# Optimization experiments

Measured on AMD Instinct MI355X. Metric: run time of the kernel, lower is better.

Reference implementation:

```python
import jax, jax.numpy as jnp
import numpy as np

NUM_USERS = 10000
NUM_ITEMS = 100000
EMBED_DIM = 64
BATCH = 4096


def setup_inputs() -> dict:
    key = jax.random.key(0)
    k1, k2, k3, k4, k5 = jax.random.split(key, 5)
    user_emb = jax.random.normal(k1, (NUM_USERS, EMBED_DIM), dtype=jnp.float32)
    item_emb = jax.random.normal(k2, (NUM_ITEMS, EMBED_DIM), dtype=jnp.float32)
    social_weight = jax.random.normal(k3, (NUM_USERS, NUM_USERS), dtype=jnp.float32)
    users = jax.random.randint(k4, (BATCH,), 0, NUM_USERS, dtype=jnp.int64)
    items = jax.random.randint(k5, (BATCH,), 0, NUM_ITEMS, dtype=jnp.int64)
    return {"user_emb": user_emb, "item_emb": item_emb,
            "social_weight": social_weight, "users": users, "items": items}


def reference(user_emb, item_emb, social_weight, users, items):
    # Embedding gathers
    bu = user_emb[users]            # [B, D]
    bi = item_emb[items]            # [B, D]
    # Per-sample dot product (bmm of [B,1,D] x [B,D,1] in the original)
    pos = jnp.sum(bu * bi, axis=-1)                      # [B]
    # Social branch. Original tiles user table B times and does bmm:
    #   scores[b] = user_emb @ bi[b]  -> [B, U]; one matmul, no replication.
    social_scores = jnp.einsum('bd,ud->bu', bi, user_emb)  # [B, U]
    bw = social_weight[users]                              # [B, U]
    social_influence = jnp.sum(bw * social_scores, axis=-1)  # [B]
    return pos + social_influence
```

## Files before the change

kernel.cpp:

```cpp
#include <hip/hip_runtime.h>
#include <hip/hip_bf16.h>

#define NUSERS   10000
#define NITEMS   100000
#define DIM      64
#define BATCH    4096

#define KPAD     10016
#define NSTEPS   313
#define STEPS_PER_CHUNK 16
#define NCHUNK   20
#define MT       64
#define LSTR     40

typedef __bf16 bf16_t;
typedef __bf16 bf16x8 __attribute__((ext_vector_type(8)));
typedef float  f32x4  __attribute__((ext_vector_type(4)));

__global__ void prep_ueT_kernel(const float* __restrict__ user_emb,
                                bf16_t* __restrict__ ueT) {
    int d = blockIdx.y;
    int k = blockIdx.x * 256 + threadIdx.x;
    if (k >= KPAD) return;
    float v = (k < NUSERS) ? user_emb[(size_t)k * DIM + d] : 0.0f;
    ueT[(size_t)d * KPAD + k] = (bf16_t)v;
}

__global__ void pos_kernel(const float* __restrict__ user_emb,
                           const float* __restrict__ item_emb,
                           const int* __restrict__ users,
                           const int* __restrict__ items,
                           float* __restrict__ out) {
    int w    = threadIdx.x >> 6;
    int lane = threadIdx.x & 63;
    int b    = blockIdx.x * 4 + w;
    if (b >= BATCH) return;
    int uid = users[b];
    int iid = items[b];
    float v = user_emb[(size_t)uid * DIM + lane] * item_emb[(size_t)iid * DIM + lane];
    v += __shfl_xor(v, 32, 64);
    v += __shfl_xor(v, 16, 64);
    v += __shfl_xor(v, 8, 64);
    v += __shfl_xor(v, 4, 64);
    v += __shfl_xor(v, 2, 64);
    v += __shfl_xor(v, 1, 64);
    if (lane == 0) out[b] = v;
}

__global__ __launch_bounds__(256) void social_kernel(
        const float* __restrict__ sw,
        const bf16_t* __restrict__ ueT,
        const float* __restrict__ item_emb,
        const int* __restrict__ users,
        const int* __restrict__ items,
        float* __restrict__ out) {
    __shared__ bf16_t Atile[MT * LSTR];
    __shared__ bf16_t Btile[DIM * LSTR];
    __shared__ int uid_s[MT];

    const int tid = threadIdx.x;
    const int m0  = blockIdx.y * MT;
    const int s0  = blockIdx.x * STEPS_PER_CHUNK;
    const int s1  = (s0 + STEPS_PER_CHUNK < NSTEPS) ? s0 + STEPS_PER_CHUNK : NSTEPS;

    if (tid < MT) uid_s[tid] = users[m0 + tid];
    __syncthreads();

    const int srow = tid >> 2;
    const int sseg = tid & 3;
    const size_t a_row_base = (size_t)uid_s[srow] * NUSERS;

    const int lane = tid & 63;
    const int w    = tid >> 6;
    const int q    = lane >> 4;
    const int c    = lane & 15;

    f32x4 acc0 = {0.f, 0.f, 0.f, 0.f};
    f32x4 acc1 = {0.f, 0.f, 0.f, 0.f};
    f32x4 acc2 = {0.f, 0.f, 0.f, 0.f};
    f32x4 acc3 = {0.f, 0.f, 0.f, 0.f};

    for (int s = s0; s < s1; ++s) {
        const int k0 = s * 32;
        const int ka = k0 + 8 * sseg;

        float4 a0 = {0.f, 0.f, 0.f, 0.f};
        float4 a1 = {0.f, 0.f, 0.f, 0.f};
        if (ka < NUSERS) {
            const float4* p = (const float4*)(sw + a_row_base + ka);
            a0 = p[0];
            a1 = p[1];
        }
        const bf16x8 bvec = *(const bf16x8*)(ueT + (size_t)srow * KPAD + ka);

        __syncthreads();

        bf16x8 av;
        av[0] = (bf16_t)a0.x; av[1] = (bf16_t)a0.y;
        av[2] = (bf16_t)a0.z; av[3] = (bf16_t)a0.w;
        av[4] = (bf16_t)a1.x; av[5] = (bf16_t)a1.y;
        av[6] = (bf16_t)a1.z; av[7] = (bf16_t)a1.w;
        *(bf16x8*)(Atile + srow * LSTR + 8 * sseg) = av;
        *(bf16x8*)(Btile + srow * LSTR + 8 * sseg) = bvec;

        __syncthreads();

        const bf16x8 afrag = *(const bf16x8*)(Atile + (16 * w + c) * LSTR + 8 * q);
        const bf16x8 b0 = *(const bf16x8*)(Btile + (c     ) * LSTR + 8 * q);
        const bf16x8 b1 = *(const bf16x8*)(Btile + (c + 16) * LSTR + 8 * q);
        const bf16x8 b2 = *(const bf16x8*)(Btile + (c + 32) * LSTR + 8 * q);
        const bf16x8 b3 = *(const bf16x8*)(Btile + (c + 48) * LSTR + 8 * q);

        acc0 = __builtin_amdgcn_mfma_f32_16x16x32_bf16(afrag, b0, acc0, 0, 0, 0);
        acc1 = __builtin_amdgcn_mfma_f32_16x16x32_bf16(afrag, b1, acc1, 0, 0, 0);
        acc2 = __builtin_amdgcn_mfma_f32_16x16x32_bf16(afrag, b2, acc2, 0, 0, 0);
        acc3 = __builtin_amdgcn_mfma_f32_16x16x32_bf16(afrag, b3, acc3, 0, 0, 0);
    }

    for (int r = 0; r < 4; ++r) {
        const int grow = m0 + 16 * w + 4 * q + r;
        const int iid  = items[grow];
        const float* ie = item_emb + (size_t)iid * DIM;
        float v = acc0[r] * ie[c]
                + acc1[r] * ie[c + 16]
                + acc2[r] * ie[c + 32]
                + acc3[r] * ie[c + 48];
        v += __shfl_xor(v, 1, 64);
        v += __shfl_xor(v, 2, 64);
        v += __shfl_xor(v, 4, 64);
        v += __shfl_xor(v, 8, 64);
        if (c == 0) atomicAdd(out + grow, v);
    }
}

extern "C" void kernel_launch(void* const* d_in, const int* in_sizes, int n_in,
                              void* d_out, int out_size, void* d_ws, size_t ws_size,
                              hipStream_t stream) {
    const float* user_emb = (const float*)d_in[0];
    const float* item_emb = (const float*)d_in[1];
    const float* sw       = (const float*)d_in[2];
    const int*   users    = (const int*)d_in[3];
    const int*   items    = (const int*)d_in[4];
    float* out = (float*)d_out;

    bf16_t* ueT = (bf16_t*)d_ws;

    prep_ueT_kernel<<<dim3((KPAD + 255) / 256, DIM), 256, 0, stream>>>(user_emb, ueT);

    pos_kernel<<<BATCH / 4, 256, 0, stream>>>(user_emb, item_emb, users, items, out);

    social_kernel<<<dim3(NCHUNK, BATCH / MT), 256, 0, stream>>>(
        sw, ueT, item_emb, users, items, out);
}
```

Baseline: 491.6 us.

## Load MFMA fragments directly from global memory, dropping LDS staging and barriers

The social GEMM kernel no longer stages A and B tiles in shared memory. Each lane now loads its own MFMA A fragment (the gathered social_weight row, converted to bf16) and its B fragments (the transposed bf16 user embeddings) straight from global memory, which removes both __syncthreads per step. KPAD is padded to 10240 so every chunk runs a fixed 16 steps, and the loop is unrolled by two. In exchange, each 64-wide tile of B is fetched by four waves instead of once per block, and the per-lane strided loads are less coalesced.

```diff
diff --git a/kernel.cpp b/kernel.cpp
--- a/kernel.cpp
+++ b/kernel.cpp
@@ -6,12 +6,10 @@
 #define DIM      64
 #define BATCH    4096
 
-#define KPAD     10016
-#define NSTEPS   313
-#define STEPS_PER_CHUNK 16
+#define KPAD     10240
+#define SPC      16
 #define NCHUNK   20
 #define MT       64
-#define LSTR     40
 
 typedef __bf16 bf16_t;
 typedef __bf16 bf16x8 __attribute__((ext_vector_type(8)));
@@ -21,7 +19,6 @@
                                 bf16_t* __restrict__ ueT) {
     int d = blockIdx.y;
     int k = blockIdx.x * 256 + threadIdx.x;
-    if (k >= KPAD) return;
     float v = (k < NUSERS) ? user_emb[(size_t)k * DIM + d] : 0.0f;
     ueT[(size_t)d * KPAD + k] = (bf16_t)v;
 }
@@ -54,67 +51,52 @@
         const int* __restrict__ users,
         const int* __restrict__ items,
         float* __restrict__ out) {
-    __shared__ bf16_t Atile[MT * LSTR];
-    __shared__ bf16_t Btile[DIM * LSTR];
-    __shared__ int uid_s[MT];
-
-    const int tid = threadIdx.x;
-    const int m0  = blockIdx.y * MT;
-    const int s0  = blockIdx.x * STEPS_PER_CHUNK;
-    const int s1  = (s0 + STEPS_PER_CHUNK < NSTEPS) ? s0 + STEPS_PER_CHUNK : NSTEPS;
-
-    if (tid < MT) uid_s[tid] = users[m0 + tid];
-    __syncthreads();
-
-    const int srow = tid >> 2;
-    const int sseg = tid & 3;
-    const size_t a_row_base = (size_t)uid_s[srow] * NUSERS;
-
+    const int tid  = threadIdx.x;
+    const int w    = tid >> 6;
     const int lane = tid & 63;
-    const int w    = tid >> 6;
     const int q    = lane >> 4;
     const int c    = lane & 15;
+
+    const int m0   = blockIdx.y * MT;
+    const int arow = m0 + 16 * w + c;
+    const int uid  = users[arow];
+    const float*  ap  = sw + (size_t)uid * NUSERS;
+    const bf16_t* bp0 = ueT + (size_t)(c     ) * KPAD;
+    const bf16_t* bp1 = ueT + (size_t)(c + 16) * KPAD;
+    const bf16_t* bp2 = ueT + (size_t)(c + 32) * KPAD;
+    const bf16_t* bp3 = ueT + (size_t)(c + 48) * KPAD;
 
     f32x4 acc0 = {0.f, 0.f, 0.f, 0.f};
     f32x4 acc1 = {0.f, 0.f, 0.f, 0.f};
     f32x4 acc2 = {0.f, 0.f, 0.f, 0.f};
     f32x4 acc3 = {0.f, 0.f, 0.f, 0.f};
 
-    for (int s = s0; s < s1; ++s) {
-        const int k0 = s * 32;
-        const int ka = k0 + 8 * sseg;
+    int k = blockIdx.x * (SPC * 32) + 8 * q;
 
+    #pragma unroll 2
+    for (int s = 0; s < SPC; ++s, k += 32) {
         float4 a0 = {0.f, 0.f, 0.f, 0.f};
         float4 a1 = {0.f, 0.f, 0.f, 0.f};
-        if (ka < NUSERS) {
-            const float4* p = (const float4*)(sw + a_row_base + ka);
+        if (k < NUSERS) {
+            const float4* p = (const float4*)(ap + k);
             a0 = p[0];
             a1 = p[1];
         }
-        const bf16x8 bvec = *(const bf16x8*)(ueT + (size_t)srow * KPAD + ka);
-
-        __syncthreads();
+        const bf16x8 b0 = *(const bf16x8*)(bp0 + k);
+        const bf16x8 b1 = *(const bf16x8*)(bp1 + k);
+        const bf16x8 b2 = *(const bf16x8*)(bp2 + k);
+        const bf16x8 b3 = *(const bf16x8*)(bp3 + k);
 
         bf16x8 av;
         av[0] = (bf16_t)a0.x; av[1] = (bf16_t)a0.y;
         av[2] = (bf16_t)a0.z; av[3] = (bf16_t)a0.w;
         av[4] = (bf16_t)a1.x; av[5] = (bf16_t)a1.y;
         av[6] = (bf16_t)a1.z; av[7] = (bf16_t)a1.w;
-        *(bf16x8*)(Atile + srow * LSTR + 8 * sseg) = av;
-        *(bf16x8*)(Btile + srow * LSTR + 8 * sseg) = bvec;
 
-        __syncthreads();
-
-        const bf16x8 afrag = *(const bf16x8*)(Atile + (16 * w + c) * LSTR + 8 * q);
-        const bf16x8 b0 = *(const bf16x8*)(Btile + (c     ) * LSTR + 8 * q);
-        const bf16x8 b1 = *(const bf16x8*)(Btile + (c + 16) * LSTR + 8 * q);
-        const bf16x8 b2 = *(const bf16x8*)(Btile + (c + 32) * LSTR + 8 * q);
-        const bf16x8 b3 = *(const bf16x8*)(Btile + (c + 48) * LSTR + 8 * q);
-
-        acc0 = __builtin_amdgcn_mfma_f32_16x16x32_bf16(afrag, b0, acc0, 0, 0, 0);
-        acc1 = __builtin_amdgcn_mfma_f32_16x16x32_bf16(afrag, b1, acc1, 0, 0, 0);
-        acc2 = __builtin_amdgcn_mfma_f32_16x16x32_bf16(afrag, b2, acc2, 0, 0, 0);
-        acc3 = __builtin_amdgcn_mfma_f32_16x16x32_bf16(afrag, b3, acc3, 0, 0, 0);
+        acc0 = __builtin_amdgcn_mfma_f32_16x16x32_bf16(av, b0, acc0, 0, 0, 0);
+        acc1 = __builtin_amdgcn_mfma_f32_16x16x32_bf16(av, b1, acc1, 0, 0, 0);
+        acc2 = __builtin_amdgcn_mfma_f32_16x16x32_bf16(av, b2, acc2, 0, 0, 0);
+        acc3 = __builtin_amdgcn_mfma_f32_16x16x32_bf16(av, b3, acc3, 0, 0, 0);
     }
 
     for (int r = 0; r < 4; ++r) {
@@ -145,7 +127,7 @@
 
     bf16_t* ueT = (bf16_t*)d_ws;
 
-    prep_ueT_kernel<<<dim3((KPAD + 255) / 256, DIM), 256, 0, stream>>>(user_emb, ueT);
+    prep_ueT_kernel<<<dim3(KPAD / 256, DIM), 256, 0, stream>>>(user_emb, ueT);
 
     pos_kernel<<<BATCH / 4, 256, 0, stream>>>(user_emb, item_emb, users, items, out);
 
```

New measurement: 513.1 us. 4.4% more time.
